# Performance work log

Hardware: AMD Instinct MI355X
Metric: run time of the kernel (lower is better)

## Reference

```python
import jax, jax.numpy as jnp
import numpy as np
jax.config.update("jax_enable_x64", True)

T, C, F = 2048, 2048, 8192
f32 = jnp.float32
f64 = jnp.float64


def setup_inputs() -> dict:
    key = jax.random.key(0)
    ks = jax.random.split(key, 20)
    s = 0.02
    return {
        "x": jax.random.normal(ks[0], (T, C), f32),
        "att_shift": jnp.zeros((C,), f32),
        "wkv_state": jnp.zeros((2, C), f32),
        "ffn_shift": jnp.zeros((C,), f32),
        "ln1_w": jnp.ones((C,), f32),
        "ln1_b": jnp.zeros((C,), f32),
        "ln2_w": jnp.ones((C,), f32),
        "ln2_b": jnp.zeros((C,), f32),
        "time_mix_k": jax.random.uniform(ks[1], (C,), f32),
        "time_mix_v": jax.random.uniform(ks[2], (C,), f32),
        "time_mix_r": jax.random.uniform(ks[3], (C,), f32),
        "time_decay": jax.random.normal(ks[4], (C,), f32) * 0.5,
        "time_first": jax.random.normal(ks[5], (C,), f32) * 0.5,
        "att_key": jax.random.normal(ks[6], (C, C), f32) * s,
        "att_value": jax.random.normal(ks[7], (C, C), f32) * s,
        "att_receptance": jax.random.normal(ks[8], (C, C), f32) * s,
        "att_output": jax.random.normal(ks[9], (C, C), f32) * s,
        "ffn_time_mix_k": jax.random.uniform(ks[10], (C,), f32),
        "ffn_time_mix_r": jax.random.uniform(ks[11], (C,), f32),
        "ffn_key": jax.random.normal(ks[12], (F, C), f32) * s,
        "ffn_value": jax.random.normal(ks[13], (C, F), f32) * s,
        "ffn_receptance": jax.random.normal(ks[14], (C, C), f32) * s,
    }


def _ln(x, w, b):
    m = x.mean(-1, keepdims=True)
    v = x.var(-1, keepdims=True)
    return (x - m) * jax.lax.rsqrt(v + 1e-5) * w + b


def _wkv(time_decay, time_first, k, v, wkv_state):
    # faithful to wkv_mop: double-precision math, float32 state round-trip per step
    u = time_first.astype(f64)
    w = -jnp.exp(time_decay.astype(f64))
    ew = jnp.exp(w)

    def step(carry, kv_t):
        a, b = carry  # float32 states [C]
        k_t, v_t = kv_t
        kd = k_t.astype(f64)
        vd = v_t.astype(f64)
        e = jnp.exp(u + w + kd)
        y = (a + e * vd) / (b + e)
        kk = jnp.exp(kd)
        a2 = ((a + kk * vd) * ew).astype(f32)
        b2 = ((b + kk) * ew).astype(f32)
        return (a2, b2), y.astype(f32)

    _, y = jax.lax.scan(step, (wkv_state[0], wkv_state[1]), (k, v))
    return y  # [T, C]


def reference(x, att_shift, wkv_state, ffn_shift, ln1_w, ln1_b, ln2_w, ln2_b,
              time_mix_k, time_mix_v, time_mix_r, time_decay, time_first,
              att_key, att_value, att_receptance, att_output,
              ffn_time_mix_k, ffn_time_mix_r, ffn_key, ffn_value, ffn_receptance):
    # --- TimeMix (att) on rx = ln1(x); shiftamount=2 -> prev token of rx ---
    rx = _ln(x, ln1_w, ln1_b)                         # [T, C]
    xx = jnp.concatenate([att_shift[None, :], rx[:-1]], axis=0)
    xk = rx * time_mix_k + xx * (1.0 - time_mix_k)
    xv = rx * time_mix_v + xx * (1.0 - time_mix_v)
    xr = rx * time_mix_r + xx * (1.0 - time_mix_r)
    k = xk @ att_key.T                                # [T, C]
    v = xv @ att_value.T
    sr = jax.nn.sigmoid(xr @ att_receptance.T)
    y = _wkv(time_decay, time_first, k, v, wkv_state)
    x = x + (sr * y) @ att_output.T
    # --- ChannelMix (ffn) on fx = ln2(x); shift = prev token of fx ---
    fx = _ln(x, ln2_w, ln2_b)
    fxx = jnp.concatenate([ffn_shift[None, :], fx[:-1]], axis=0)
    fk = fx * ffn_time_mix_k + fxx * (1.0 - ffn_time_mix_k)
    fr = fx * ffn_time_mix_r + fxx * (1.0 - ffn_time_mix_r)
    kf = jnp.square(jax.nn.relu(fk @ ffn_key.T))      # [T, F]
    kv = kf @ ffn_value.T                             # [T, C]
    out = x + jax.nn.sigmoid(fr @ ffn_receptance.T) * kv
    return out
```

## Files before the change

### kernel.cpp

```cpp
#include <hip/hip_runtime.h>
#include <hip/hip_bf16.h>

typedef unsigned short u16;
typedef short bf16x8 __attribute__((ext_vector_type(8)));
typedef float f32x4 __attribute__((ext_vector_type(4)));

#define T_DIM 2048
#define C_DIM 2048
#define F_DIM 8192
#define WKV_L 32
#define WKV_P (T_DIM / WKV_L)

__device__ __forceinline__ u16 f2bf(float f) {
    unsigned int u = __float_as_uint(f);
    u += 0x7fff + ((u >> 16) & 1);
    return (u16)(u >> 16);
}

__device__ __forceinline__ void async16(const void* g, void* l) {
    __builtin_amdgcn_global_load_lds(
        (__attribute__((address_space(1))) const unsigned int*)g,
        (__attribute__((address_space(3))) unsigned int*)l, 16, 0, 0);
}

__global__ __launch_bounds__(256) void ln_mix3(
        const float* __restrict__ x, const float* __restrict__ sh,
        const float* __restrict__ w, const float* __restrict__ b,
        const float* __restrict__ mk, const float* __restrict__ mv,
        const float* __restrict__ mr,
        u16* __restrict__ xk, u16* __restrict__ xv, u16* __restrict__ xr) {
    __shared__ float red[16];
    const int t = blockIdx.x, tid = threadIdx.x;
    const float4* cr = (const float4*)(x + (size_t)t * C_DIM);
    float4 c0 = cr[tid * 2], c1 = cr[tid * 2 + 1];
    float s = c0.x + c0.y + c0.z + c0.w + c1.x + c1.y + c1.z + c1.w;
    float q = c0.x * c0.x + c0.y * c0.y + c0.z * c0.z + c0.w * c0.w
            + c1.x * c1.x + c1.y * c1.y + c1.z * c1.z + c1.w * c1.w;
    float4 p0, p1;
    float sp = 0.f, qp = 0.f;
    if (t > 0) {
        const float4* pr = (const float4*)(x + (size_t)(t - 1) * C_DIM);
        p0 = pr[tid * 2]; p1 = pr[tid * 2 + 1];
        sp = p0.x + p0.y + p0.z + p0.w + p1.x + p1.y + p1.z + p1.w;
        qp = p0.x * p0.x + p0.y * p0.y + p0.z * p0.z + p0.w * p0.w
           + p1.x * p1.x + p1.y * p1.y + p1.z * p1.z + p1.w * p1.w;
    } else {
        const float4* pr = (const float4*)sh;
        p0 = pr[tid * 2]; p1 = pr[tid * 2 + 1];
    }
    #pragma unroll
    for (int off = 32; off > 0; off >>= 1) {
        s += __shfl_down(s, off);   q += __shfl_down(q, off);
        sp += __shfl_down(sp, off); qp += __shfl_down(qp, off);
    }
    const int lane = tid & 63, wv = tid >> 6;
    if (lane == 0) { red[wv] = s; red[4 + wv] = q; red[8 + wv] = sp; red[12 + wv] = qp; }
    __syncthreads();
    if (tid == 0) {
        red[0] += red[1] + red[2] + red[3];
        red[4] += red[5] + red[6] + red[7];
        red[8] += red[9] + red[10] + red[11];
        red[12] += red[13] + red[14] + red[15];
    }
    __syncthreads();
    const float mc = red[0] * (1.f / C_DIM);
    const float ic = rsqrtf(red[4] * (1.f / C_DIM) - mc * mc + 1e-5f);
    const float mp = red[8] * (1.f / C_DIM);
    const float ip = rsqrtf(red[12] * (1.f / C_DIM) - mp * mp + 1e-5f);
    const float4* w4 = (const float4*)w;
    const float4* b4 = (const float4*)b;
    #pragma unroll
    for (int j = 0; j < 2; ++j) {
        const int i4 = tid * 2 + j;
        float4 cv = j ? c1 : c0, pv = j ? p1 : p0;
        float4 wv4 = w4[i4], bv = b4[i4];
        float4 cl, pl;
        cl.x = (cv.x - mc) * ic * wv4.x + bv.x;
        cl.y = (cv.y - mc) * ic * wv4.y + bv.y;
        cl.z = (cv.z - mc) * ic * wv4.z + bv.z;
        cl.w = (cv.w - mc) * ic * wv4.w + bv.w;
        if (t > 0) {
            pl.x = (pv.x - mp) * ip * wv4.x + bv.x;
            pl.y = (pv.y - mp) * ip * wv4.y + bv.y;
            pl.z = (pv.z - mp) * ip * wv4.z + bv.z;
            pl.w = (pv.w - mp) * ip * wv4.w + bv.w;
        } else pl = pv;
        const size_t o = (size_t)t * (C_DIM / 4) + i4;
        float4 m;
        ushort4 r;
        m = ((const float4*)mk)[i4];
        r.x = f2bf(cl.x * m.x + pl.x * (1.f - m.x));
        r.y = f2bf(cl.y * m.y + pl.y * (1.f - m.y));
        r.z = f2bf(cl.z * m.z + pl.z * (1.f - m.z));
        r.w = f2bf(cl.w * m.w + pl.w * (1.f - m.w));
        ((ushort4*)xk)[o] = r;
        m = ((const float4*)mv)[i4];
        r.x = f2bf(cl.x * m.x + pl.x * (1.f - m.x));
        r.y = f2bf(cl.y * m.y + pl.y * (1.f - m.y));
        r.z = f2bf(cl.z * m.z + pl.z * (1.f - m.z));
        r.w = f2bf(cl.w * m.w + pl.w * (1.f - m.w));
        ((ushort4*)xv)[o] = r;
        m = ((const float4*)mr)[i4];
        r.x = f2bf(cl.x * m.x + pl.x * (1.f - m.x));
        r.y = f2bf(cl.y * m.y + pl.y * (1.f - m.y));
        r.z = f2bf(cl.z * m.z + pl.z * (1.f - m.z));
        r.w = f2bf(cl.w * m.w + pl.w * (1.f - m.w));
        ((ushort4*)xr)[o] = r;
    }
}

__global__ __launch_bounds__(256) void ln_mix2(
        const float* __restrict__ x, const float* __restrict__ sh,
        const float* __restrict__ w, const float* __restrict__ b,
        const float* __restrict__ mk, const float* __restrict__ mr,
        u16* __restrict__ fk, u16* __restrict__ fr) {
    __shared__ float red[16];
    const int t = blockIdx.x, tid = threadIdx.x;
    const float4* cr = (const float4*)(x + (size_t)t * C_DIM);
    float4 c0 = cr[tid * 2], c1 = cr[tid * 2 + 1];
    float s = c0.x + c0.y + c0.z + c0.w + c1.x + c1.y + c1.z + c1.w;
    float q = c0.x * c0.x + c0.y * c0.y + c0.z * c0.z + c0.w * c0.w
            + c1.x * c1.x + c1.y * c1.y + c1.z * c1.z + c1.w * c1.w;
    float4 p0, p1;
    float sp = 0.f, qp = 0.f;
    if (t > 0) {
        const float4* pr = (const float4*)(x + (size_t)(t - 1) * C_DIM);
        p0 = pr[tid * 2]; p1 = pr[tid * 2 + 1];
        sp = p0.x + p0.y + p0.z + p0.w + p1.x + p1.y + p1.z + p1.w;
        qp = p0.x * p0.x + p0.y * p0.y + p0.z * p0.z + p0.w * p0.w
           + p1.x * p1.x + p1.y * p1.y + p1.z * p1.z + p1.w * p1.w;
    } else {
        const float4* pr = (const float4*)sh;
        p0 = pr[tid * 2]; p1 = pr[tid * 2 + 1];
    }
    #pragma unroll
    for (int off = 32; off > 0; off >>= 1) {
        s += __shfl_down(s, off);   q += __shfl_down(q, off);
        sp += __shfl_down(sp, off); qp += __shfl_down(qp, off);
    }
    const int lane = tid & 63, wv = tid >> 6;
    if (lane == 0) { red[wv] = s; red[4 + wv] = q; red[8 + wv] = sp; red[12 + wv] = qp; }
    __syncthreads();
    if (tid == 0) {
        red[0] += red[1] + red[2] + red[3];
        red[4] += red[5] + red[6] + red[7];
        red[8] += red[9] + red[10] + red[11];
        red[12] += red[13] + red[14] + red[15];
    }
    __syncthreads();
    const float mc = red[0] * (1.f / C_DIM);
    const float ic = rsqrtf(red[4] * (1.f / C_DIM) - mc * mc + 1e-5f);
    const float mp = red[8] * (1.f / C_DIM);
    const float ip = rsqrtf(red[12] * (1.f / C_DIM) - mp * mp + 1e-5f);
    const float4* w4 = (const float4*)w;
    const float4* b4 = (const float4*)b;
    #pragma unroll
    for (int j = 0; j < 2; ++j) {
        const int i4 = tid * 2 + j;
        float4 cv = j ? c1 : c0, pv = j ? p1 : p0;
        float4 wv4 = w4[i4], bv = b4[i4];
        float4 cl, pl;
        cl.x = (cv.x - mc) * ic * wv4.x + bv.x;
        cl.y = (cv.y - mc) * ic * wv4.y + bv.y;
        cl.z = (cv.z - mc) * ic * wv4.z + bv.z;
        cl.w = (cv.w - mc) * ic * wv4.w + bv.w;
        if (t > 0) {
            pl.x = (pv.x - mp) * ip * wv4.x + bv.x;
            pl.y = (pv.y - mp) * ip * wv4.y + bv.y;
            pl.z = (pv.z - mp) * ip * wv4.z + bv.z;
            pl.w = (pv.w - mp) * ip * wv4.w + bv.w;
        } else pl = pv;
        const size_t o = (size_t)t * (C_DIM / 4) + i4;
        float4 m;
        ushort4 r;
        m = ((const float4*)mk)[i4];
        r.x = f2bf(cl.x * m.x + pl.x * (1.f - m.x));
        r.y = f2bf(cl.y * m.y + pl.y * (1.f - m.y));
        r.z = f2bf(cl.z * m.z + pl.z * (1.f - m.z));
        r.w = f2bf(cl.w * m.w + pl.w * (1.f - m.w));
        ((ushort4*)fk)[o] = r;
        m = ((const float4*)mr)[i4];
        r.x = f2bf(cl.x * m.x + pl.x * (1.f - m.x));
        r.y = f2bf(cl.y * m.y + pl.y * (1.f - m.y));
        r.z = f2bf(cl.z * m.z + pl.z * (1.f - m.z));
        r.w = f2bf(cl.w * m.w + pl.w * (1.f - m.w));
        ((ushort4*)fr)[o] = r;
    }
}

__global__ __launch_bounds__(256) void cvt_bf16(const float* __restrict__ in,
                                                u16* __restrict__ out, int n8) {
    int i = blockIdx.x * 256 + threadIdx.x;
    const int stride = gridDim.x * 256;
    for (; i < n8; i += stride) {
        const float4* p = (const float4*)(in + (size_t)i * 8);
        float4 a = p[0], b = p[1];
        ushort4 lo, hi;
        lo.x = f2bf(a.x); lo.y = f2bf(a.y); lo.z = f2bf(a.z); lo.w = f2bf(a.w);
        hi.x = f2bf(b.x); hi.y = f2bf(b.y); hi.z = f2bf(b.z); hi.w = f2bf(b.w);
        ((ushort4*)out)[i * 2] = lo;
        ((ushort4*)out)[i * 2 + 1] = hi;
    }
}

__global__ __launch_bounds__(256) void cvt4_bf16(const float* __restrict__ i0,
                                                 const float* __restrict__ i1,
                                                 const float* __restrict__ i2,
                                                 const float* __restrict__ i3,
                                                 u16* __restrict__ out, int n8) {
    const int sel = blockIdx.y;
    const float* in = sel == 0 ? i0 : (sel == 1 ? i1 : (sel == 2 ? i2 : i3));
    u16* o = out + (size_t)sel * n8 * 8;
    int i = blockIdx.x * 256 + threadIdx.x;
    const int stride = gridDim.x * 256;
    for (; i < n8; i += stride) {
        const float4* p = (const float4*)(in + (size_t)i * 8);
        float4 a = p[0], b = p[1];
        ushort4 lo, hi;
        lo.x = f2bf(a.x); lo.y = f2bf(a.y); lo.z = f2bf(a.z); lo.w = f2bf(a.w);
        hi.x = f2bf(b.x); hi.y = f2bf(b.y); hi.z = f2bf(b.z); hi.w = f2bf(b.w);
        ((ushort4*)o)[i * 2] = lo;
        ((ushort4*)o)[i * 2 + 1] = hi;
    }
}

__global__ __launch_bounds__(256) void reduce4(const float* __restrict__ p0,
                                               const float* __restrict__ p1,
                                               const float* __restrict__ p2,
                                               const float* __restrict__ p3,
                                               float* __restrict__ o, int n4) {
    int i = blockIdx.x * 256 + threadIdx.x;
    const int stride = gridDim.x * 256;
    for (; i < n4; i += stride) {
        float4 a = ((const float4*)p0)[i], b = ((const float4*)p1)[i];
        float4 c = ((const float4*)p2)[i], d = ((const float4*)p3)[i];
        float4 r;
        r.x = a.x + b.x + c.x + d.x;
        r.y = a.y + b.y + c.y + d.y;
        r.z = a.z + b.z + c.z + d.z;
        r.w = a.w + b.w + c.w + d.w;
        ((float4*)o)[i] = r;
    }
}

__global__ __launch_bounds__(256) void wkv_part(const float* __restrict__ td,
                                                const float* __restrict__ k,
                                                const float* __restrict__ v,
                                                float* __restrict__ Ab,
                                                float* __restrict__ Bb) {
    const int idx = blockIdx.x * 256 + threadIdx.x;
    const int c = idx & (C_DIM - 1);
    const int p = idx >> 11;
    const float ew = expf(-expf(td[c]));
    float A = 0.f, B = 0.f;
    size_t o = (size_t)(p * WKV_L) * C_DIM + c;
    #pragma unroll 4
    for (int i = 0; i < WKV_L; ++i, o += C_DIM) {
        const float kk = expf(k[o]);
        A = (A + kk * v[o]) * ew;
        B = (B + kk) * ew;
    }
    Ab[p * C_DIM + c] = A;
    Bb[p * C_DIM + c] = B;
}

__global__ __launch_bounds__(256) void wkv_comb(const float* __restrict__ td,
                                                const float* __restrict__ st,
                                                const float* __restrict__ Ab,
                                                const float* __restrict__ Bb,
                                                float* __restrict__ Sa,
                                                float* __restrict__ Sb) {
    const int c = blockIdx.x * 256 + threadIdx.x;
    const float w = -expf(td[c]);
    const float dL = expf(w * (float)WKV_L);
    float a = st[c];
    float b = st[C_DIM + c];
    #pragma unroll 4
    for (int p = 0; p < WKV_P; ++p) {
        Sa[p * C_DIM + c] = a;
        Sb[p * C_DIM + c] = b;
        a = dL * a + Ab[p * C_DIM + c];
        b = dL * b + Bb[p * C_DIM + c];
    }
}

__global__ __launch_bounds__(256) void wkv_emit(const float* __restrict__ td,
                                                const float* __restrict__ tf,
                                                const float* __restrict__ k,
                                                const float* __restrict__ v,
                                                const float* __restrict__ r,
                                                const float* __restrict__ Sa,
                                                const float* __restrict__ Sb,
                                                u16* __restrict__ pout) {
    const int idx = blockIdx.x * 256 + threadIdx.x;
    const int c = idx & (C_DIM - 1);
    const int p = idx >> 11;
    const float u = tf[c];
    const float w = -expf(td[c]);
    const float ew = expf(w);
    float a = Sa[p * C_DIM + c];
    float b = Sb[p * C_DIM + c];
    size_t o = (size_t)(p * WKV_L) * C_DIM + c;
    #pragma unroll 2
    for (int i = 0; i < WKV_L; ++i, o += C_DIM) {
        const float kt = k[o], vt = v[o], rt = r[o];
        const float e = expf(u + w + kt);
        const float y = (a + e * vt) / (b + e);
        const float kk = expf(kt);
        a = (a + kk * vt) * ew;
        b = (b + kk) * ew;
        const float sr = 1.f / (1.f + expf(-rt));
        pout[o] = f2bf(sr * y);
    }
}

enum { EPI_F32 = 0, EPI_ADDX = 1, EPI_RELU2 = 2, EPI_SIGMULADD = 3 };

template <int EPI>
__global__ __launch_bounds__(256, 3) void gemm_bt(
        const u16* __restrict__ A, int lda, long a_zs,
        const u16* __restrict__ B, int ldb, long b_zs,
        long koff, int Kloop,
        void* __restrict__ outp, int ldo, long o_zs,
        const float* __restrict__ aux1, const float* __restrict__ aux2) {
    __shared__ u16 lds[3 * 8192];
    const int tid = threadIdx.x;
    const int l = tid & 63, w = tid >> 6;
    const int wr2 = w >> 1, wc2 = w & 1;

    const int gx = gridDim.x, gy = gridDim.y;
    const int nxy = gx * gy;
    const int flat = (blockIdx.z * gy + blockIdx.y) * gx + blockIdx.x;
    const int cpx = (nxy * gridDim.z) >> 3;
    const int swz = (flat & 7) * cpx + (flat >> 3);
    const int z = swz / nxy;
    const int rem = swz - z * nxy;
    const int bm = rem % gy;
    const int bn = rem / gy;

    const u16* Ag = A + (size_t)z * a_zs + (size_t)z * koff + (size_t)bm * 128 * lda;
    const u16* Bg = B + (size_t)z * b_zs + (size_t)z * koff + (size_t)bn * 128 * ldb;

    long gA[2], gB[2];
    int dA[2], dB[2];
    #pragma unroll
    for (int j = 0; j < 2; ++j) {
        const int off = j * 4096 + w * 1024 + l * 16;
        const int row = off >> 6;
        const int cb = (off & 63) ^ (((off >> 9) & 1) << 5);
        gA[j] = (long)row * lda + (cb >> 1);
        gB[j] = (long)row * ldb + (cb >> 1);
        dA[j] = j * 2048 + w * 512;
        dB[j] = 4096 + j * 2048 + w * 512;
    }

    int offA[4], offB[4];
    #pragma unroll
    for (int m = 0; m < 4; ++m) {
        const int lin = (wr2 * 64 + m * 16 + (l & 15)) * 64 + ((l >> 4) << 4);
        offA[m] = (lin ^ (((lin >> 9) & 1) << 5)) >> 1;
    }
    #pragma unroll
    for (int n = 0; n < 4; ++n) {
        const int lin = (wc2 * 64 + n * 16 + (l & 15)) * 64 + ((l >> 4) << 4);
        offB[n] = 4096 + ((lin ^ (((lin >> 9) & 1) << 5)) >> 1);
    }

    const f32x4 fz = {0.f, 0.f, 0.f, 0.f};
    f32x4 acc[4][4];
    #pragma unroll
    for (int m = 0; m < 4; ++m)
        #pragma unroll
        for (int n = 0; n < 4; ++n) acc[m][n] = fz;

    const int NT = Kloop >> 5;

    auto stage = [&](int kt, int sp) {
        const long ko = (long)kt << 5;
        const int sb = sp * 8192;
        async16(Ag + gA[0] + ko, &lds[sb + dA[0]]);
        async16(Ag + gA[1] + ko, &lds[sb + dA[1]]);
        async16(Bg + gB[0] + ko, &lds[sb + dB[0]]);
        async16(Bg + gB[1] + ko, &lds[sb + dB[1]]);
    };

    stage(0, 0);
    stage(1, 1);

    int sr = 0;
    for (int t = 0; t < NT; ++t) {
        asm volatile("s_waitcnt vmcnt(4)" ::: "memory");
        __builtin_amdgcn_s_barrier();
        __builtin_amdgcn_sched_barrier(0);
        {
            const int tp = (t + 2 < NT) ? t + 2 : NT - 1;
            const int sp = (sr == 0) ? 2 : sr - 1;
            stage(tp, sp);
        }
        const int sb = sr * 8192;
        bf16x8 af[4], bfv[4];
        #pragma unroll
        for (int m = 0; m < 4; ++m) af[m] = *(const bf16x8*)&lds[sb + offA[m]];
        #pragma unroll
        for (int n = 0; n < 4; ++n) bfv[n] = *(const bf16x8*)&lds[sb + offB[n]];
        __builtin_amdgcn_s_setprio(1);
        #pragma unroll
        for (int m = 0; m < 2; ++m)
            #pragma unroll
            for (int n = 0; n < 4; ++n)
                acc[m][n] = __builtin_amdgcn_mfma_f32_16x16x32_bf16(af[m], bfv[n], acc[m][n], 0, 0, 0);
        __builtin_amdgcn_s_setprio(0);
        __builtin_amdgcn_s_setprio(1);
        #pragma unroll
        for (int m = 2; m < 4; ++m)
            #pragma unroll
            for (int n = 0; n < 4; ++n)
                acc[m][n] = __builtin_amdgcn_mfma_f32_16x16x32_bf16(af[m], bfv[n], acc[m][n], 0, 0, 0);
        __builtin_amdgcn_s_setprio(0);
        sr = (sr == 2) ? 0 : sr + 1;
    }
    asm volatile("s_waitcnt vmcnt(0)" ::: "memory");

    const int r00 = bm * 128 + wr2 * 64 + ((l >> 4) << 2);
    const int c00 = bn * 128 + wc2 * 64 + (l & 15);
    #pragma unroll
    for (int m = 0; m < 4; ++m) {
        #pragma unroll
        for (int n = 0; n < 4; ++n) {
            #pragma unroll
            for (int j = 0; j < 4; ++j) {
                const int rr = r00 + m * 16 + j;
                const int cc = c00 + n * 16;
                const size_t o = (size_t)rr * ldo + cc;
                const float val = acc[m][n][j];
                if constexpr (EPI == EPI_F32) {
                    ((float*)outp)[(size_t)z * o_zs + o] = val;
                } else if constexpr (EPI == EPI_ADDX) {
                    ((float*)outp)[o] = aux1[o] + val;
                } else if constexpr (EPI == EPI_RELU2) {
                    const float tp2 = fmaxf(val, 0.f);
                    ((u16*)outp)[o] = f2bf(tp2 * tp2);
                } else {
                    const float sg = 1.f / (1.f + expf(-val));
                    ((float*)outp)[o] = aux1[o] + sg * aux2[o];
                }
            }
        }
    }
}

template <int EPI>
__global__ __launch_bounds__(512, 2) void gemm8p(
        const u16* __restrict__ A, int lda,
        const u16* __restrict__ B, int ldb,
        long koff, int Kloop,
        void* __restrict__ outp, int ldo, long o_zs) {
    __shared__ u16 lds[65536];
    const int tid = threadIdx.x;
    const int l = tid & 63, w = tid >> 6;
    const int wm = w >> 2, wn = w & 3;

    const int gx = gridDim.x, gy = gridDim.y;
    const int nxy = gx * gy;
    const int flat = (blockIdx.z * gy + blockIdx.y) * gx + blockIdx.x;
    const int cpx = (nxy * gridDim.z) >> 3;
    const int swz = (flat & 7) * cpx + (flat >> 3);
    const int z = swz / nxy;
    const int rem = swz - z * nxy;
    const int bm = rem % gy;
    const int bn = rem / gy;

    const u16* Ag = A + (size_t)z * koff + (size_t)bm * 256 * lda;
    const u16* Bg = B + (size_t)z * koff + (size_t)bn * 256 * ldb;

    long srcA[4], srcB[4];
    int dst[4];
    #pragma unroll
    for (int hj = 0; hj < 4; ++hj) {
        const int off = (hj >> 1) * 16384 + (hj & 1) * 8192 + w * 1024 + l * 16;
        const int e = off ^ (((off >> 7) & 7) << 4);
        srcA[hj] = (long)(e >> 7) * lda + ((e & 127) >> 1);
        srcB[hj] = (long)(e >> 7) * ldb + ((e & 127) >> 1);
        dst[hj] = off >> 1;
    }

    int offA[2][4], offB0[4];
    #pragma unroll
    for (int mh = 0; mh < 2; ++mh)
        #pragma unroll
        for (int mi = 0; mi < 4; ++mi) {
            const int row = wm * 128 + (mh * 4 + mi) * 16 + (l & 15);
            const int lin = row * 128 + ((l >> 4) << 4);
            offA[mh][mi] = (lin ^ (((lin >> 7) & 7) << 4)) >> 1;
        }
    #pragma unroll
    for (int n = 0; n < 4; ++n) {
        const int row = wn * 64 + n * 16 + (l & 15);
        const int lin = row * 128 + ((l >> 4) << 4);
        offB0[n] = 16384 + ((lin ^ (((lin >> 7) & 7) << 4)) >> 1);
    }

    const f32x4 fz = {0.f, 0.f, 0.f, 0.f};
    f32x4 acc[8][4];
    #pragma unroll
    for (int m = 0; m < 8; ++m)
        #pragma unroll
        for (int n = 0; n < 4; ++n) acc[m][n] = fz;

    const int NT = Kloop >> 6;
    const int NP = NT >> 1;

    auto stgA = [&](int kt, int buf, int h) {
        const long ko = (long)kt << 6;
        #pragma unroll
        for (int j = 0; j < 2; ++j)
            async16(Ag + srcA[h * 2 + j] + ko, &lds[buf * 32768 + dst[h * 2 + j]]);
    };
    auto stgB = [&](int kt, int buf, int h) {
        const long ko = (long)kt << 6;
        #pragma unroll
        for (int j = 0; j < 2; ++j)
            async16(Bg + srcB[h * 2 + j] + ko, &lds[buf * 32768 + 16384 + dst[h * 2 + j]]);
    };

#define PH_OPEN() __builtin_amdgcn_s_barrier(); \
    asm volatile("s_waitcnt lgkmcnt(0)" ::: "memory"); \
    __builtin_amdgcn_sched_barrier(0)
#define QUAD(af, bf, MO) \
    __builtin_amdgcn_s_setprio(1); \
    _Pragma("unroll") \
    for (int mi = 0; mi < 4; ++mi) \
        _Pragma("unroll") \
        for (int n = 0; n < 4; ++n) \
            acc[MO + mi][n] = __builtin_amdgcn_mfma_f32_16x16x32_bf16((af)[mi], (bf)[n], acc[MO + mi][n], 0, 0, 0); \
    __builtin_amdgcn_s_setprio(0)

    stgA(0, 0, 0); stgA(0, 0, 1); stgB(0, 0, 0); stgB(0, 0, 1);
    stgA(1, 1, 0);
    asm volatile("s_waitcnt vmcnt(2)" ::: "memory");
    __builtin_amdgcn_s_barrier();

    for (int p = 0; p < NP; ++p) {
        const int kt1 = 2 * p + 1;
        const int kn0 = (2 * p + 2 < NT) ? 2 * p + 2 : NT - 1;
        const int kn1 = (2 * p + 3 < NT) ? 2 * p + 3 : NT - 1;
        bf16x8 a0[4], a1[4], a0k[4], a1k[4], bb[4];
        #pragma unroll
        for (int mi = 0; mi < 4; ++mi) a0[mi] = *(const bf16x8*)&lds[offA[0][mi]];
        #pragma unroll
        for (int n = 0; n < 4; ++n) bb[n] = *(const bf16x8*)&lds[offB0[n]];
        stgA(kt1, 1, 1);
        PH_OPEN(); QUAD(a0, bb, 0);
        __builtin_amdgcn_s_barrier();
        #pragma unroll
        for (int mi = 0; mi < 4; ++mi) a1[mi] = *(const bf16x8*)&lds[offA[1][mi]];
        #pragma unroll
        for (int mi = 0; mi < 4; ++mi) a0k[mi] = *(const bf16x8*)&lds[offA[0][mi] ^ 32];
        stgB(kt1, 1, 0);
        PH_OPEN(); QUAD(a1, bb, 4);
        __builtin_amdgcn_s_barrier();
        #pragma unroll
        for (int n = 0; n < 4; ++n) bb[n] = *(const bf16x8*)&lds[offB0[n] ^ 32];
        #pragma unroll
        for (int mi = 0; mi < 4; ++mi) a1k[mi] = *(const bf16x8*)&lds[offA[1][mi] ^ 32];
        stgB(kt1, 1, 1);
        PH_OPEN(); QUAD(a0k, bb, 0);
        __builtin_amdgcn_s_barrier();
        stgA(kn0, 0, 0);
        PH_OPEN(); QUAD(a1k, bb, 4);
        asm volatile("s_waitcnt vmcnt(2)" ::: "memory");
        __builtin_amdgcn_s_barrier();
        #pragma unroll
        for (int mi = 0; mi < 4; ++mi) a0[mi] = *(const bf16x8*)&lds[32768 + offA[0][mi]];
        #pragma unroll
        for (int n = 0; n < 4; ++n) bb[n] = *(const bf16x8*)&lds[32768 + offB0[n]];
        stgA(kn0, 0, 1);
        PH_OPEN(); QUAD(a0, bb, 0);
        __builtin_amdgcn_s_barrier();
        #pragma unroll
        for (int mi = 0; mi < 4; ++mi) a1[mi] = *(const bf16x8*)&lds[32768 + offA[1][mi]];
        #pragma unroll
        for (int mi = 0; mi < 4; ++mi) a0k[mi] = *(const bf16x8*)&lds[32768 + (offA[0][mi] ^ 32)];
        stgB(kn0, 0, 0);
        PH_OPEN(); QUAD(a1, bb, 4);
        __builtin_amdgcn_s_barrier();
        #pragma unroll
        for (int n = 0; n < 4; ++n) bb[n] = *(const bf16x8*)&lds[32768 + (offB0[n] ^ 32)];
        #pragma unroll
        for (int mi = 0; mi < 4; ++mi) a1k[mi] = *(const bf16x8*)&lds[32768 + (offA[1][mi] ^ 32)];
        stgB(kn0, 0, 1);
        PH_OPEN(); QUAD(a0k, bb, 0);
        __builtin_amdgcn_s_barrier();
        stgA(kn1, 1, 0);
        PH_OPEN(); QUAD(a1k, bb, 4);
        asm volatile("s_waitcnt vmcnt(2)" ::: "memory");
        __builtin_amdgcn_s_barrier();
    }
    asm volatile("s_waitcnt vmcnt(0)" ::: "memory");

#undef PH_OPEN
#undef QUAD

    const int r00 = bm * 256 + wm * 128 + ((l >> 4) << 2);
    const int c00 = bn * 256 + wn * 64 + (l & 15);
    #pragma unroll
    for (int m = 0; m < 8; ++m) {
        #pragma unroll
        for (int n = 0; n < 4; ++n) {
            #pragma unroll
            for (int j = 0; j < 4; ++j) {
                const int rr = r00 + m * 16 + j;
                const int cc = c00 + n * 16;
                const size_t o = (size_t)rr * ldo + cc;
                const float val = acc[m][n][j];
                if constexpr (EPI == EPI_F32) {
                    ((float*)outp)[(size_t)z * o_zs + o] = val;
                } else {
                    const float tp2 = fmaxf(val, 0.f);
                    ((u16*)outp)[o] = f2bf(tp2 * tp2);
                }
            }
        }
    }
}

extern "C" void kernel_launch(void* const* d_in, const int* in_sizes, int n_in,
                              void* d_out, int out_size, void* d_ws, size_t ws_size,
                              hipStream_t stream) {
    const float* x         = (const float*)d_in[0];
    const float* att_shift = (const float*)d_in[1];
    const float* wkv_state = (const float*)d_in[2];
    const float* ffn_shift = (const float*)d_in[3];
    const float* ln1w = (const float*)d_in[4];
    const float* ln1b = (const float*)d_in[5];
    const float* ln2w = (const float*)d_in[6];
    const float* ln2b = (const float*)d_in[7];
    const float* tmk  = (const float*)d_in[8];
    const float* tmv  = (const float*)d_in[9];
    const float* tmr  = (const float*)d_in[10];
    const float* td   = (const float*)d_in[11];
    const float* tf   = (const float*)d_in[12];
    const float* Wk   = (const float*)d_in[13];
    const float* Wv   = (const float*)d_in[14];
    const float* Wr   = (const float*)d_in[15];
    const float* Wo   = (const float*)d_in[16];
    const float* ftmk = (const float*)d_in[17];
    const float* ftmr = (const float*)d_in[18];
    const float* Wfk  = (const float*)d_in[19];
    const float* Wfv  = (const float*)d_in[20];
    const float* Wfr  = (const float*)d_in[21];
    float* out = (float*)d_out;

    char* ws = (char*)d_ws;
    const size_t MB = 1ull << 20;
    float* rx0 = (float*)(ws + 0);
    u16*   xk  = (u16*)(ws + 16 * MB);
    u16*   xv  = (u16*)(ws + 24 * MB);
    u16*   xr  = (u16*)(ws + 32 * MB);
    float* kb  = (float*)(ws + 40 * MB);
    float* vb  = (float*)(ws + 56 * MB);
    float* rb  = (float*)(ws + 72 * MB);
    u16*   pb  = (u16*)(ws + 88 * MB);
    float* x1  = (float*)(ws + 96 * MB);
    u16*   kf  = (u16*)(ws + 112 * MB);
    u16*   Wb  = (u16*)(ws + 144 * MB);
    float* wAb = (float*)(ws + 112 * MB);
    float* wBb = (float*)(ws + 112 * MB + 512 * 1024);
    float* wSa = (float*)(ws + 113 * MB);
    float* wSb = (float*)(ws + 113 * MB + 512 * 1024);
    float* fvp = (float*)(ws + 32 * MB);

    const int T = T_DIM, C = C_DIM, F = F_DIM;
    const dim3 blk(256), blk5(512);

    ln_mix3<<<T, blk, 0, stream>>>(x, att_shift, ln1w, ln1b, tmk, tmv, tmr, xk, xv, xr);

    cvt4_bf16<<<dim3(1024, 4), blk, 0, stream>>>(Wk, Wv, Wr, Wo, Wb, C * C / 8);
    gemm_bt<EPI_F32><<<dim3(C / 128, T / 128, 3), blk, 0, stream>>>(
        xk, C, (long)T * C, Wb, C, (long)C * C, 0, C,
        kb, C, (long)T * C, nullptr, nullptr);

    wkv_part<<<(C * WKV_P) / 256, blk, 0, stream>>>(td, kb, vb, wAb, wBb);
    wkv_comb<<<C / 256, blk, 0, stream>>>(td, wkv_state, wAb, wBb, wSa, wSb);
    wkv_emit<<<(C * WKV_P) / 256, blk, 0, stream>>>(td, tf, kb, vb, rb, wSa, wSb, pb);

    gemm_bt<EPI_ADDX><<<dim3(C / 128, T / 128, 1), blk, 0, stream>>>(
        pb, C, 0, Wb + 3 * (size_t)C * C, C, 0, 0, C, x1, C, 0, x, nullptr);

    ln_mix2<<<T, blk, 0, stream>>>(x1, ffn_shift, ln2w, ln2b, ftmk, ftmr, xk, xv);

    cvt_bf16<<<2048, blk, 0, stream>>>(Wfk, Wb, F * C / 8);
    gemm8p<EPI_RELU2><<<dim3(F / 256, T / 256, 1), blk5, 0, stream>>>(
        xk, C, Wb, C, 0, C, kf, F, 0);

    cvt_bf16<<<2048, blk, 0, stream>>>(Wfv, Wb, C * F / 8);
    gemm8p<EPI_F32><<<dim3(C / 256, T / 256, 4), blk5, 0, stream>>>(
        kf, F, Wb, F, 2048, 2048, fvp, C, (long)T * C);
    reduce4<<<2048, blk, 0, stream>>>(fvp, fvp + (size_t)T * C, fvp + 2 * (size_t)T * C,
                                      fvp + 3 * (size_t)T * C, rx0, T * C / 4);

    cvt_bf16<<<2048, blk, 0, stream>>>(Wfr, Wb, C * C / 8);
    gemm_bt<EPI_SIGMULADD><<<dim3(C / 128, T / 128, 1), blk, 0, stream>>>(
        xv, C, 0, Wb, C, 0, 0, C, out, C, 0, x1, rx0);
}
```

Before: 383.6 us.

## Replace double-buffered K=64 GEMM pipeline with triple-buffered K=32 stages

The FFN GEMM kernel moves from two 64-wide K stages in 128 KB of LDS to three 32-wide K stages in 96 KB, with a new XOR swizzle for the 64-byte rows. The loop now preloads the next tile's fragments in registers while issuing the MFMAs for the current one, and keeps two global loads in flight ahead. This aims to hide global-load latency and cut LDS use, which may raise occupancy. In exchange there are more barriers per unit of K, and the hand-tuned waitcnt counts must be exactly right to stay correct.

```diff
diff --git a/kernel.cpp b/kernel.cpp
--- a/kernel.cpp
+++ b/kernel.cpp
@@ -450,12 +450,12 @@
 }
 
 template <int EPI>
-__global__ __launch_bounds__(512, 2) void gemm8p(
+__global__ __launch_bounds__(512, 2) void gemm3s(
         const u16* __restrict__ A, int lda,
         const u16* __restrict__ B, int ldb,
         long koff, int Kloop,
         void* __restrict__ outp, int ldo, long o_zs) {
-    __shared__ u16 lds[65536];
+    __shared__ u16 lds[3 * 16384];
     const int tid = threadIdx.x;
     const int l = tid & 63, w = tid >> 6;
     const int wm = w >> 2, wn = w & 3;
@@ -464,40 +464,42 @@
     const int nxy = gx * gy;
     const int flat = (blockIdx.z * gy + blockIdx.y) * gx + blockIdx.x;
     const int cpx = (nxy * gridDim.z) >> 3;
-    const int swz = (flat & 7) * cpx + (flat >> 3);
-    const int z = swz / nxy;
-    const int rem = swz - z * nxy;
+    const int swzb = (flat & 7) * cpx + (flat >> 3);
+    const int z = swzb / nxy;
+    const int rem = swzb - z * nxy;
     const int bm = rem % gy;
     const int bn = rem / gy;
 
     const u16* Ag = A + (size_t)z * koff + (size_t)bm * 256 * lda;
     const u16* Bg = B + (size_t)z * koff + (size_t)bn * 256 * ldb;
 
-    long srcA[4], srcB[4];
-    int dst[4];
-    #pragma unroll
-    for (int hj = 0; hj < 4; ++hj) {
-        const int off = (hj >> 1) * 16384 + (hj & 1) * 8192 + w * 1024 + l * 16;
-        const int e = off ^ (((off >> 7) & 7) << 4);
-        srcA[hj] = (long)(e >> 7) * lda + ((e & 127) >> 1);
-        srcB[hj] = (long)(e >> 7) * ldb + ((e & 127) >> 1);
-        dst[hj] = off >> 1;
-    }
-
-    int offA[2][4], offB0[4];
-    #pragma unroll
-    for (int mh = 0; mh < 2; ++mh)
-        #pragma unroll
-        for (int mi = 0; mi < 4; ++mi) {
-            const int row = wm * 128 + (mh * 4 + mi) * 16 + (l & 15);
-            const int lin = row * 128 + ((l >> 4) << 4);
-            offA[mh][mi] = (lin ^ (((lin >> 7) & 7) << 4)) >> 1;
-        }
+    long srcA[2], srcB[2];
+    int dstA[2], dstB[2];
+    #pragma unroll
+    for (int h = 0; h < 2; ++h) {
+        const int off = h * 8192 + w * 1024 + l * 16;
+        const int row = off >> 6;
+        const int cbyte = (off & 63) ^ (((off >> 9) & 1) << 5);
+        srcA[h] = (long)row * lda + (cbyte >> 1);
+        srcB[h] = (long)row * ldb + (cbyte >> 1);
+        dstA[h] = off >> 1;
+        dstB[h] = 8192 + (off >> 1);
+    }
+
+    int offAL[4], offAH[4], offB[4];
+    #pragma unroll
+    for (int mi = 0; mi < 4; ++mi) {
+        int row = wm * 128 + mi * 16 + (l & 15);
+        int lin = row * 64 + ((l >> 4) << 4);
+        offAL[mi] = (lin ^ (((lin >> 9) & 1) << 5)) >> 1;
+        lin = (row + 64) * 64 + ((l >> 4) << 4);
+        offAH[mi] = (lin ^ (((lin >> 9) & 1) << 5)) >> 1;
+    }
     #pragma unroll
     for (int n = 0; n < 4; ++n) {
         const int row = wn * 64 + n * 16 + (l & 15);
-        const int lin = row * 128 + ((l >> 4) << 4);
-        offB0[n] = 16384 + ((lin ^ (((lin >> 7) & 7) << 4)) >> 1);
+        const int lin = row * 64 + ((l >> 4) << 4);
+        offB[n] = 8192 + ((lin ^ (((lin >> 9) & 1) << 5)) >> 1);
     }
 
     const f32x4 fz = {0.f, 0.f, 0.f, 0.f};
@@ -507,99 +509,71 @@
         #pragma unroll
         for (int n = 0; n < 4; ++n) acc[m][n] = fz;
 
-    const int NT = Kloop >> 6;
-    const int NP = NT >> 1;
+    const int NT = Kloop >> 5;
 
     auto stgA = [&](int kt, int buf, int h) {
-        const long ko = (long)kt << 6;
-        #pragma unroll
-        for (int j = 0; j < 2; ++j)
-            async16(Ag + srcA[h * 2 + j] + ko, &lds[buf * 32768 + dst[h * 2 + j]]);
+        async16(Ag + srcA[h] + (long)kt * 32, &lds[buf * 16384 + dstA[h]]);
     };
     auto stgB = [&](int kt, int buf, int h) {
-        const long ko = (long)kt << 6;
-        #pragma unroll
-        for (int j = 0; j < 2; ++j)
-            async16(Bg + srcB[h * 2 + j] + ko, &lds[buf * 32768 + 16384 + dst[h * 2 + j]]);
+        async16(Bg + srcB[h] + (long)kt * 32, &lds[buf * 16384 + dstB[h]]);
     };
 
-#define PH_OPEN() __builtin_amdgcn_s_barrier(); \
-    asm volatile("s_waitcnt lgkmcnt(0)" ::: "memory"); \
-    __builtin_amdgcn_sched_barrier(0)
-#define QUAD(af, bf, MO) \
-    __builtin_amdgcn_s_setprio(1); \
-    _Pragma("unroll") \
-    for (int mi = 0; mi < 4; ++mi) \
-        _Pragma("unroll") \
-        for (int n = 0; n < 4; ++n) \
-            acc[MO + mi][n] = __builtin_amdgcn_mfma_f32_16x16x32_bf16((af)[mi], (bf)[n], acc[MO + mi][n], 0, 0, 0); \
-    __builtin_amdgcn_s_setprio(0)
-
     stgA(0, 0, 0); stgA(0, 0, 1); stgB(0, 0, 0); stgB(0, 0, 1);
-    stgA(1, 1, 0);
-    asm volatile("s_waitcnt vmcnt(2)" ::: "memory");
+    stgA(1, 1, 0); stgA(1, 1, 1); stgB(1, 1, 0); stgB(1, 1, 1);
+    asm volatile("s_waitcnt vmcnt(4)" ::: "memory");
     __builtin_amdgcn_s_barrier();
 
-    for (int p = 0; p < NP; ++p) {
-        const int kt1 = 2 * p + 1;
-        const int kn0 = (2 * p + 2 < NT) ? 2 * p + 2 : NT - 1;
-        const int kn1 = (2 * p + 3 < NT) ? 2 * p + 3 : NT - 1;
-        bf16x8 a0[4], a1[4], a0k[4], a1k[4], bb[4];
-        #pragma unroll
-        for (int mi = 0; mi < 4; ++mi) a0[mi] = *(const bf16x8*)&lds[offA[0][mi]];
-        #pragma unroll
-        for (int n = 0; n < 4; ++n) bb[n] = *(const bf16x8*)&lds[offB0[n]];
-        stgA(kt1, 1, 1);
-        PH_OPEN(); QUAD(a0, bb, 0);
+    bf16x8 aX[4], bX[4], aY[4], bY[4];
+    #pragma unroll
+    for (int mi = 0; mi < 4; ++mi) aX[mi] = *(const bf16x8*)&lds[offAL[mi]];
+    #pragma unroll
+    for (int n = 0; n < 4; ++n) bX[n] = *(const bf16x8*)&lds[offB[n]];
+
+    auto tile = [&](int kt, bf16x8 (&aC)[4], bf16x8 (&bbC)[4],
+                    bf16x8 (&aN)[4], bf16x8 (&bbN)[4]) {
+        const int cb = (kt % 3) * 16384;
+        const int nb = ((kt + 1) % 3) * 16384;
+        const int tb = (kt + 2) % 3;
+        const int ksrc = (kt + 2 < NT) ? kt + 2 : NT - 1;
+        bf16x8 aH[4];
+        #pragma unroll
+        for (int mi = 0; mi < 4; ++mi) aH[mi] = *(const bf16x8*)&lds[cb + offAH[mi]];
+        stgA(ksrc, tb, 0); stgA(ksrc, tb, 1);
         __builtin_amdgcn_s_barrier();
-        #pragma unroll
-        for (int mi = 0; mi < 4; ++mi) a1[mi] = *(const bf16x8*)&lds[offA[1][mi]];
-        #pragma unroll
-        for (int mi = 0; mi < 4; ++mi) a0k[mi] = *(const bf16x8*)&lds[offA[0][mi] ^ 32];
-        stgB(kt1, 1, 0);
-        PH_OPEN(); QUAD(a1, bb, 4);
-        __builtin_amdgcn_s_barrier();
-        #pragma unroll
-        for (int n = 0; n < 4; ++n) bb[n] = *(const bf16x8*)&lds[offB0[n] ^ 32];
-        #pragma unroll
-        for (int mi = 0; mi < 4; ++mi) a1k[mi] = *(const bf16x8*)&lds[offA[1][mi] ^ 32];
-        stgB(kt1, 1, 1);
-        PH_OPEN(); QUAD(a0k, bb, 0);
-        __builtin_amdgcn_s_barrier();
-        stgA(kn0, 0, 0);
-        PH_OPEN(); QUAD(a1k, bb, 4);
+        asm volatile("s_waitcnt lgkmcnt(4)" ::: "memory");
+        __builtin_amdgcn_sched_barrier(0);
+        __builtin_amdgcn_s_setprio(1);
+        #pragma unroll
+        for (int mi = 0; mi < 4; ++mi)
+            #pragma unroll
+            for (int n = 0; n < 4; ++n)
+                acc[mi][n] = __builtin_amdgcn_mfma_f32_16x16x32_bf16(aC[mi], bbC[n], acc[mi][n], 0, 0, 0);
+        __builtin_amdgcn_s_setprio(0);
         asm volatile("s_waitcnt vmcnt(2)" ::: "memory");
         __builtin_amdgcn_s_barrier();
         #pragma unroll
-        for (int mi = 0; mi < 4; ++mi) a0[mi] = *(const bf16x8*)&lds[32768 + offA[0][mi]];
-        #pragma unroll
-        for (int n = 0; n < 4; ++n) bb[n] = *(const bf16x8*)&lds[32768 + offB0[n]];
-        stgA(kn0, 0, 1);
-        PH_OPEN(); QUAD(a0, bb, 0);
+        for (int mi = 0; mi < 4; ++mi) aN[mi] = *(const bf16x8*)&lds[nb + offAL[mi]];
+        #pragma unroll
+        for (int n = 0; n < 4; ++n) bbN[n] = *(const bf16x8*)&lds[nb + offB[n]];
+        stgB(ksrc, tb, 0); stgB(ksrc, tb, 1);
         __builtin_amdgcn_s_barrier();
-        #pragma unroll
-        for (int mi = 0; mi < 4; ++mi) a1[mi] = *(const bf16x8*)&lds[32768 + offA[1][mi]];
-        #pragma unroll
-        for (int mi = 0; mi < 4; ++mi) a0k[mi] = *(const bf16x8*)&lds[32768 + (offA[0][mi] ^ 32)];
-        stgB(kn0, 0, 0);
-        PH_OPEN(); QUAD(a1, bb, 4);
+        asm volatile("s_waitcnt lgkmcnt(8)" ::: "memory");
+        __builtin_amdgcn_sched_barrier(0);
+        __builtin_amdgcn_s_setprio(1);
+        #pragma unroll
+        for (int mi = 0; mi < 4; ++mi)
+            #pragma unroll
+            for (int n = 0; n < 4; ++n)
+                acc[4 + mi][n] = __builtin_amdgcn_mfma_f32_16x16x32_bf16(aH[mi], bbC[n], acc[4 + mi][n], 0, 0, 0);
+        __builtin_amdgcn_s_setprio(0);
         __builtin_amdgcn_s_barrier();
-        #pragma unroll
-        for (int n = 0; n < 4; ++n) bb[n] = *(const bf16x8*)&lds[32768 + (offB0[n] ^ 32)];
-        #pragma unroll
-        for (int mi = 0; mi < 4; ++mi) a1k[mi] = *(const bf16x8*)&lds[32768 + (offA[1][mi] ^ 32)];
-        stgB(kn0, 0, 1);
-        PH_OPEN(); QUAD(a0k, bb, 0);
-        __builtin_amdgcn_s_barrier();
-        stgA(kn1, 1, 0);
-        PH_OPEN(); QUAD(a1k, bb, 4);
-        asm volatile("s_waitcnt vmcnt(2)" ::: "memory");
-        __builtin_amdgcn_s_barrier();
+    };
+
+    for (int kt = 0; kt < NT; kt += 2) {
+        tile(kt, aX, bX, aY, bY);
+        tile(kt + 1, aY, bY, aX, bX);
     }
     asm volatile("s_waitcnt vmcnt(0)" ::: "memory");
-
-#undef PH_OPEN
-#undef QUAD
 
     const int r00 = bm * 256 + wm * 128 + ((l >> 4) << 2);
     const int c00 = bn * 256 + wn * 64 + (l & 15);
@@ -690,11 +664,11 @@
     ln_mix2<<<T, blk, 0, stream>>>(x1, ffn_shift, ln2w, ln2b, ftmk, ftmr, xk, xv);
 
     cvt_bf16<<<2048, blk, 0, stream>>>(Wfk, Wb, F * C / 8);
-    gemm8p<EPI_RELU2><<<dim3(F / 256, T / 256, 1), blk5, 0, stream>>>(
+    gemm3s<EPI_RELU2><<<dim3(F / 256, T / 256, 1), blk5, 0, stream>>>(
         xk, C, Wb, C, 0, C, kf, F, 0);
 
     cvt_bf16<<<2048, blk, 0, stream>>>(Wfv, Wb, C * F / 8);
-    gemm8p<EPI_F32><<<dim3(C / 256, T / 256, 4), blk5, 0, stream>>>(
+    gemm3s<EPI_F32><<<dim3(C / 256, T / 256, 4), blk5, 0, stream>>>(
         kf, F, Wb, F, 2048, 2048, fvp, C, (long)T * C);
     reduce4<<<2048, blk, 0, stream>>>(fvp, fvp + (size_t)T * C, fvp + 2 * (size_t)T * C,
                                       fvp + 3 * (size_t)T * C, rx0, T * C / 4);
```

New measurement: 391.2 us. No clear change (+2.0%).
